# Kernel tuning notes

Measured on AMD Instinct MI355X. Metric: run time of the kernel, lower is better.

The kernel has to match this reference:

```python
import jax, jax.numpy as jnp
import numpy as np

EPS = 1e-6  # torch.nn.functional.pairwise_distance default eps (added elementwise before the norm)


def setup_inputs() -> dict:
    key = jax.random.key(0)
    k1, k2, k3 = jax.random.split(key, 3)
    N, D, K = 4096, 128, 512
    net_out = jax.random.normal(k1, (N, D), dtype=jnp.float32)
    label = jax.random.randint(k2, (N,), 0, K, dtype=jnp.int64)
    # xavier_normal_ with gain=1 on a (D, K) tensor: std = sqrt(2 / (fan_in + fan_out))
    std = np.sqrt(2.0 / (D + K)).astype(np.float32)
    w = jax.random.normal(k3, (D, K), dtype=jnp.float32) * std
    return {"net_out": net_out, "label": label, "w": w}


def reference(net_out, label, w):
    # scores[n, k] = -||net_out[n, :] - w[:, k] + eps||_2   (norm over repr_dim, as in the
    # torch-1.x pairwise_distance with inputs expanded to N x D x K, reduced over dim=1)
    diff = net_out[:, :, None] - w[None, :, :] + EPS  # (N, D, K)
    scores = -jnp.sqrt(jnp.sum(diff * diff, axis=1))  # (N, K)
    # nn.CrossEntropyLoss: mean over batch of -log_softmax(scores)[n, label[n]]
    logp = jax.nn.log_softmax(scores, axis=-1)
    loss = -jnp.mean(jnp.take_along_axis(logp, label[:, None], axis=1))
    return (scores, loss)
```

## Files before the change

kernel.cpp:

```cpp
#include <hip/hip_runtime.h>
#include <hip/hip_bf16.h>
#include <math.h>

#define N_ROWS 4096
#define D_DIM  128
#define K_CLS  512
#define RPB    16
#define NBLK   (N_ROWS / RPB)

typedef __attribute__((ext_vector_type(8))) short short8v;
typedef __attribute__((ext_vector_type(4))) float f32x4;

__device__ __forceinline__ short f2bf_rne(float v) {
    return (short)__bfloat16_as_ushort(__float2bfloat16(v));
}

__global__ __launch_bounds__(1024) void proto_main_kernel(
    const float* __restrict__ x,
    const int*   __restrict__ label,
    const float* __restrict__ w,
    float* __restrict__ scores,
    float* __restrict__ row_loss)
{
    const int tid  = threadIdx.x;
    const int wave = tid >> 6;
    const int lane = tid & 63;
    const int l15  = lane & 15;
    const int q    = lane >> 4;
    const int n0   = blockIdx.x * RPB;

    __shared__ float wm[16][16];
    __shared__ float we[16][16];
    __shared__ float gm[16];
    __shared__ float slab[RPB];

    short8v afrag[4];
    float p = 0.f;
#pragma unroll
    for (int t = 0; t < 4; ++t) {
        const int row = n0 + l15;
        const int d0  = t * 32 + q * 8;
        const float4 a = *(const float4*)&x[(size_t)row * D_DIM + d0];
        const float4 b = *(const float4*)&x[(size_t)row * D_DIM + d0 + 4];
        p = fmaf(a.x, a.x, p); p = fmaf(a.y, a.y, p);
        p = fmaf(a.z, a.z, p); p = fmaf(a.w, a.w, p);
        p = fmaf(b.x, b.x, p); p = fmaf(b.y, b.y, p);
        p = fmaf(b.z, b.z, p); p = fmaf(b.w, b.w, p);
        short8v f;
        f[0] = f2bf_rne(a.x); f[1] = f2bf_rne(a.y);
        f[2] = f2bf_rne(a.z); f[3] = f2bf_rne(a.w);
        f[4] = f2bf_rne(b.x); f[5] = f2bf_rne(b.y);
        f[6] = f2bf_rne(b.z); f[7] = f2bf_rne(b.w);
        afrag[t] = f;
    }
    p += __shfl_xor(p, 16);
    p += __shfl_xor(p, 32);
    float sxr[4];
#pragma unroll
    for (int j = 0; j < 4; ++j) sxr[j] = __shfl(p, q * 4 + j);

    f32x4 acc[2];
    float ck[2];
    const int colbase = wave * 32;
#pragma unroll
    for (int c = 0; c < 2; ++c) {
        acc[c] = (f32x4){0.f, 0.f, 0.f, 0.f};
        float s2 = 0.f;
        const int col = colbase + c * 16 + l15;
#pragma unroll
        for (int t = 0; t < 4; ++t) {
            short8v bf;
#pragma unroll
            for (int j = 0; j < 8; ++j) {
                const float v = w[(size_t)(t * 32 + q * 8 + j) * K_CLS + col];
                s2 = fmaf(v, v, s2);
                bf[j] = f2bf_rne(v);
            }
            acc[c] = __builtin_amdgcn_mfma_f32_16x16x32_bf16(afrag[t], bf, acc[c], 0, 0, 0);
        }
        s2 += __shfl_xor(s2, 16);
        s2 += __shfl_xor(s2, 32);
        ck[c] = s2;
    }

    float sv[2][4];
#pragma unroll
    for (int c = 0; c < 2; ++c) {
        const int col = colbase + c * 16 + l15;
#pragma unroll
        for (int j = 0; j < 4; ++j) {
            const int row = q * 4 + j;
            const float dist = sxr[j] + ck[c] - 2.f * acc[c][j];
            sv[c][j] = -sqrtf(dist);
            scores[(size_t)(n0 + row) * K_CLS + col] = sv[c][j];
        }
    }

#pragma unroll
    for (int j = 0; j < 4; ++j) {
        float m = fmaxf(sv[0][j], sv[1][j]);
        m = fmaxf(m, __shfl_xor(m, 1));
        m = fmaxf(m, __shfl_xor(m, 2));
        m = fmaxf(m, __shfl_xor(m, 4));
        m = fmaxf(m, __shfl_xor(m, 8));
        if (l15 == 0) wm[wave][q * 4 + j] = m;
    }
    __syncthreads();
    if (tid < 16) {
        float g = wm[0][tid];
#pragma unroll
        for (int ww = 1; ww < 16; ++ww) g = fmaxf(g, wm[ww][tid]);
        gm[tid] = g;
    }
    __syncthreads();

#pragma unroll
    for (int j = 0; j < 4; ++j) {
        const int row = q * 4 + j;
        const float m = gm[row];
        const int lab = label[n0 + row];
        float e = 0.f;
#pragma unroll
        for (int c = 0; c < 2; ++c) {
            e += expf(sv[c][j] - m);
            if ((colbase + c * 16 + l15) == lab) slab[row] = sv[c][j];
        }
        e += __shfl_xor(e, 1);
        e += __shfl_xor(e, 2);
        e += __shfl_xor(e, 4);
        e += __shfl_xor(e, 8);
        if (l15 == 0) we[wave][row] = e;
    }
    __syncthreads();
    if (tid < RPB) {
        float es = we[0][tid];
#pragma unroll
        for (int ww = 1; ww < 16; ++ww) es += we[ww][tid];
        row_loss[n0 + tid] = -(slab[tid] - gm[tid] - logf(es));
    }
}

__global__ __launch_bounds__(256) void loss_reduce_kernel(
    const float* __restrict__ row_loss, float* __restrict__ out)
{
    __shared__ float red[4];
    const int tid = threadIdx.x;
    float sum = 0.f;
    for (int i = tid; i < N_ROWS; i += 256) sum += row_loss[i];
#pragma unroll
    for (int off = 32; off >= 1; off >>= 1) sum += __shfl_xor(sum, off);
    if ((tid & 63) == 0) red[tid >> 6] = sum;
    __syncthreads();
    if (tid == 0)
        out[0] = (red[0] + red[1] + red[2] + red[3]) * (1.0f / N_ROWS);
}

extern "C" void kernel_launch(void* const* d_in, const int* in_sizes, int n_in,
                              void* d_out, int out_size, void* d_ws, size_t ws_size,
                              hipStream_t stream)
{
    const float* x     = (const float*)d_in[0];
    const int*   label = (const int*)d_in[1];
    const float* w     = (const float*)d_in[2];

    float* scores   = (float*)d_out;
    float* loss_out = (float*)d_out + (size_t)N_ROWS * K_CLS;
    float* row_loss = (float*)d_ws;

    proto_main_kernel<<<NBLK, 1024, 0, stream>>>(x, label, w, scores, row_loss);
    loss_reduce_kernel<<<1, 256, 0, stream>>>(row_loss, loss_out);
}
```

Baseline: 21.80 us.

## Pre-pack W into bf16 MFMA fragment layout and precompute column norms in prep kernel

Adds a small prep kernel that converts W once to bf16 in the exact per-lane MFMA B-fragment order, and precomputes the per-class norm term, now with an eps correction. The main kernel then loads each B fragment with one 16-byte vector load instead of 8 strided scalar float loads plus conversion in each of 256 blocks, and drops the per-block norm shuffle reductions. The cost is an extra kernel launch and a workspace round trip.

```diff
diff --git a/kernel.cpp b/kernel.cpp
--- a/kernel.cpp
+++ b/kernel.cpp
@@ -5,6 +5,7 @@
 #define N_ROWS 4096
 #define D_DIM  128
 #define K_CLS  512
+#define EPS    1e-6f
 #define RPB    16
 #define NBLK   (N_ROWS / RPB)
 
@@ -13,12 +14,50 @@
 
 __device__ __forceinline__ short f2bf_rne(float v) {
     return (short)__bfloat16_as_ushort(__float2bfloat16(v));
+}
+
+__global__ __launch_bounds__(256) void prep_kernel(
+    const float* __restrict__ w,
+    unsigned short* __restrict__ bpk,
+    float* __restrict__ c_arr)
+{
+    const int b   = blockIdx.x;
+    const int tid = threadIdx.x;
+    if (b < 32) {
+        const int gtid = b * 256 + tid;
+        const int lane = gtid & 63;
+        const int c    = (gtid >> 6) & 31;
+        const int t    = gtid >> 11;
+        const int col  = c * 16 + (lane & 15);
+        const int d0   = t * 32 + ((lane >> 4) << 3);
+        unsigned short v[8];
+#pragma unroll
+        for (int j = 0; j < 8; ++j)
+            v[j] = (unsigned short)f2bf_rne(w[(d0 + j) * K_CLS + col]);
+        uint4 out;
+        out.x = v[0] | ((unsigned)v[1] << 16);
+        out.y = v[2] | ((unsigned)v[3] << 16);
+        out.z = v[4] | ((unsigned)v[5] << 16);
+        out.w = v[6] | ((unsigned)v[7] << 16);
+        *(uint4*)&bpk[(size_t)gtid * 8] = out;
+    } else {
+        const int k = (b - 32) * 256 + tid;
+        float s1 = 0.f, s2 = 0.f;
+#pragma unroll 8
+        for (int d = 0; d < D_DIM; ++d) {
+            const float v = w[d * K_CLS + k];
+            s1 += v;
+            s2 = fmaf(v, v, s2);
+        }
+        c_arr[k] = s2 - 2.f * EPS * s1;
+    }
 }
 
 __global__ __launch_bounds__(1024) void proto_main_kernel(
     const float* __restrict__ x,
     const int*   __restrict__ label,
-    const float* __restrict__ w,
+    const unsigned short* __restrict__ bpk,
+    const float* __restrict__ c_arr,
     float* __restrict__ scores,
     float* __restrict__ row_loss)
 {
@@ -65,22 +104,14 @@
 #pragma unroll
     for (int c = 0; c < 2; ++c) {
         acc[c] = (f32x4){0.f, 0.f, 0.f, 0.f};
-        float s2 = 0.f;
-        const int col = colbase + c * 16 + l15;
+        const int ctile = wave * 2 + c;
+        ck[c] = c_arr[ctile * 16 + l15];
 #pragma unroll
         for (int t = 0; t < 4; ++t) {
-            short8v bf;
-#pragma unroll
-            for (int j = 0; j < 8; ++j) {
-                const float v = w[(size_t)(t * 32 + q * 8 + j) * K_CLS + col];
-                s2 = fmaf(v, v, s2);
-                bf[j] = f2bf_rne(v);
-            }
+            const short8v bf =
+                *(const short8v*)&bpk[(((size_t)t * 32 + ctile) * 64 + lane) * 8];
             acc[c] = __builtin_amdgcn_mfma_f32_16x16x32_bf16(afrag[t], bf, acc[c], 0, 0, 0);
         }
-        s2 += __shfl_xor(s2, 16);
-        s2 += __shfl_xor(s2, 32);
-        ck[c] = s2;
     }
 
     float sv[2][4];
@@ -165,8 +196,13 @@
 
     float* scores   = (float*)d_out;
     float* loss_out = (float*)d_out + (size_t)N_ROWS * K_CLS;
-    float* row_loss = (float*)d_ws;
-
-    proto_main_kernel<<<NBLK, 1024, 0, stream>>>(x, label, w, scores, row_loss);
+
+    unsigned short* bpk = (unsigned short*)d_ws;
+    float* c_arr    = (float*)((char*)d_ws + 131072);
+    float* row_loss = (float*)((char*)d_ws + 133120);
+
+    prep_kernel<<<34, 256, 0, stream>>>(w, bpk, c_arr);
+    proto_main_kernel<<<NBLK, 1024, 0, stream>>>(x, label, bpk, c_arr,
+                                                 scores, row_loss);
     loss_reduce_kernel<<<1, 256, 0, stream>>>(row_loss, loss_out);
 }
```

After: 24.65 us. 1.13x slower.

## Fuse loss reduction into main kernel using ticket flags and block-0 spin wait

Applied to the files above, without the earlier changes.

Removes the second loss-reduce launch. Each block now reduces its per-row losses inside the block, takes a monotonic ticket from a global counter and publishes its partial sum with a flag. Block 0 spins on all flags, using ticket windows so the workspace works across repeated calls without a reset, then writes the mean loss. This saves a kernel launch and the gap between launches, but block 0 must wait for every other block to finish. That relies on all 256 blocks being co-resident or scheduled forward, and adds atomics and spinning.

```diff
diff --git a/kernel.cpp b/kernel.cpp
--- a/kernel.cpp
+++ b/kernel.cpp
@@ -7,6 +7,7 @@
 #define K_CLS  512
 #define RPB    16
 #define NBLK   (N_ROWS / RPB)
+#define TICKET_OFS 0x40000000u
 
 typedef __attribute__((ext_vector_type(8))) short short8v;
 typedef __attribute__((ext_vector_type(4))) float f32x4;
@@ -20,7 +21,10 @@
     const int*   __restrict__ label,
     const float* __restrict__ w,
     float* __restrict__ scores,
-    float* __restrict__ row_loss)
+    float* __restrict__ loss_out,
+    unsigned int* __restrict__ part,
+    unsigned int* __restrict__ flag,
+    unsigned int* __restrict__ cnt)
 {
     const int tid  = threadIdx.x;
     const int wave = tid >> 6;
@@ -33,6 +37,8 @@
     __shared__ float we[16][16];
     __shared__ float gm[16];
     __shared__ float slab[RPB];
+    __shared__ float red2[16];
+    __shared__ unsigned int myticket;
 
     short8v afrag[4];
     float p = 0.f;
@@ -132,27 +138,55 @@
         if (l15 == 0) we[wave][row] = e;
     }
     __syncthreads();
+
+    float bp = 0.f;
     if (tid < RPB) {
         float es = we[0][tid];
 #pragma unroll
         for (int ww = 1; ww < 16; ++ww) es += we[ww][tid];
-        row_loss[n0 + tid] = -(slab[tid] - gm[tid] - logf(es));
-    }
-}
-
-__global__ __launch_bounds__(256) void loss_reduce_kernel(
-    const float* __restrict__ row_loss, float* __restrict__ out)
-{
-    __shared__ float red[4];
-    const int tid = threadIdx.x;
-    float sum = 0.f;
-    for (int i = tid; i < N_ROWS; i += 256) sum += row_loss[i];
-#pragma unroll
-    for (int off = 32; off >= 1; off >>= 1) sum += __shfl_xor(sum, off);
-    if ((tid & 63) == 0) red[tid >> 6] = sum;
-    __syncthreads();
-    if (tid == 0)
-        out[0] = (red[0] + red[1] + red[2] + red[3]) * (1.0f / N_ROWS);
+        bp = -(slab[tid] - gm[tid] - logf(es));
+    }
+    if (wave == 0) {
+        bp += __shfl_xor(bp, 1);
+        bp += __shfl_xor(bp, 2);
+        bp += __shfl_xor(bp, 4);
+        bp += __shfl_xor(bp, 8);
+        if (lane == 0) {
+            const unsigned int old = atomicAdd(cnt, 1u);
+            atomicExch(&part[blockIdx.x], __float_as_uint(bp));
+            asm volatile("s_waitcnt vmcnt(0)" ::: "memory");
+            atomicExch(&flag[blockIdx.x], old + TICKET_OFS);
+            myticket = old + TICKET_OFS;
+        }
+    }
+
+    if (blockIdx.x == 0) {
+        __syncthreads();
+        const unsigned int lo = myticket - 255u;
+        float v = 0.f;
+        if (tid < NBLK) {
+            unsigned int f;
+            int iters = 0;
+            do {
+                f = atomicAdd(&flag[tid], 0u);
+            } while ((f - lo) > 510u && ++iters < (1 << 26));
+            v = __uint_as_float(atomicAdd(&part[tid], 0u));
+        }
+        v += __shfl_xor(v, 1);
+        v += __shfl_xor(v, 2);
+        v += __shfl_xor(v, 4);
+        v += __shfl_xor(v, 8);
+        v += __shfl_xor(v, 16);
+        v += __shfl_xor(v, 32);
+        if (lane == 0) red2[wave] = v;
+        __syncthreads();
+        if (tid == 0) {
+            float tot = 0.f;
+#pragma unroll
+            for (int ww = 0; ww < 4; ++ww) tot += red2[ww];
+            loss_out[0] = tot * (1.0f / N_ROWS);
+        }
+    }
 }
 
 extern "C" void kernel_launch(void* const* d_in, const int* in_sizes, int n_in,
@@ -165,8 +199,11 @@
 
     float* scores   = (float*)d_out;
     float* loss_out = (float*)d_out + (size_t)N_ROWS * K_CLS;
-    float* row_loss = (float*)d_ws;
-
-    proto_main_kernel<<<NBLK, 1024, 0, stream>>>(x, label, w, scores, row_loss);
-    loss_reduce_kernel<<<1, 256, 0, stream>>>(row_loss, loss_out);
+
+    unsigned int* part = (unsigned int*)d_ws;
+    unsigned int* flag = part + NBLK;
+    unsigned int* cnt  = flag + NBLK;
+
+    proto_main_kernel<<<NBLK, 1024, 0, stream>>>(x, label, w, scores, loss_out,
+                                                 part, flag, cnt);
 }
```

Result: faster. 20.18 us (-7.4%).
